# Kernel tuning notes

Measured on AMD Instinct MI355X. Metric: run time of the kernel, lower is better.

## Reference

```python
import jax, jax.numpy as jnp
import numpy as np

BS, SEQ, DIM, DIM_MLP, E = 2, 2048, 1024, 4096, 8
STD = 0.02  # nn.init.normal_(weight, std=0.02)


def setup_inputs() -> dict:
    key = jax.random.key(0)
    k_x, k_idx, k_w1, k_w2 = jax.random.split(key, 4)
    x = jax.random.normal(k_x, (BS, SEQ, DIM), dtype=jnp.float32)
    expert_idx = jax.random.randint(k_idx, (BS, SEQ), 0, E, dtype=jnp.int32)
    W1 = jax.random.normal(k_w1, (E, DIM, DIM_MLP), dtype=jnp.float32) * STD
    b1 = jnp.zeros((E, DIM_MLP), dtype=jnp.float32)
    W2 = jax.random.normal(k_w2, (E, DIM_MLP, DIM), dtype=jnp.float32) * STD
    b2 = jnp.zeros((E, DIM), dtype=jnp.float32)
    return {"x": x, "expert_idx": expert_idx, "W1": W1, "b1": b1, "W2": W2, "b2": b2}


def reference(x, expert_idx, W1, b1, W2, b2):
    # Compute ALL experts on all tokens (faithful to the torch module).
    # h: [bs, seq, E, dim_mlp]
    h = jnp.einsum("bsd,edm->bsem", x, W1) + b1
    h = jax.nn.gelu(h, approximate=False)  # torch nn.GELU default = exact erf
    # feat: [bs, seq, E, dim]  (== torch.cat along feature dim, reshaped)
    feat = jnp.einsum("bsem,emd->bsed", h, W2) + b2
    # Per-token gather of the assigned expert's output (top-1 select).
    idx = expert_idx.astype(jnp.int32)[:, :, None, None]  # [bs, seq, 1, 1]
    out = jnp.take_along_axis(feat, idx, axis=2)[:, :, 0, :]  # [bs, seq, dim]
    return out
```

## Files before the change

kernel.cpp:

```cpp
#include <hip/hip_runtime.h>
#include <hip/hip_bf16.h>
#include <math.h>

#define TOK   4096
#define DIM   1024
#define DMLP  4096
#define NE    8
#define BM    128
#define BN    128
#define BN2   64
#define BK    32
#define PADMAX (TOK + NE * BM)
#define NTILES (PADMAX / BM)

typedef __attribute__((ext_vector_type(8))) short  short8;
typedef __attribute__((ext_vector_type(4))) float  float4v;
typedef __attribute__((ext_vector_type(4))) unsigned short ushort4v;

static __device__ __forceinline__ unsigned short f2bf(float f) {
  unsigned u = __float_as_uint(f);
  u += 0x7fffu + ((u >> 16) & 1u);
  return (unsigned short)(u >> 16);
}

__global__ void group_kernel(const int* __restrict__ eidx,
                             int* __restrict__ perm,
                             int* __restrict__ tile_e) {
  __shared__ int cnt[NE], off[NE], len[NE], cur[NE];
  const int tid = threadIdx.x;
  if (tid < NE) cnt[tid] = 0;
  __syncthreads();
  for (int i = tid; i < TOK; i += 256) atomicAdd(&cnt[eidx[i]], 1);
  __syncthreads();
  if (tid == 0) {
    int o = 0;
    for (int e = 0; e < NE; e++) {
      off[e] = o;
      len[e] = ((cnt[e] + BM - 1) / BM) * BM;
      cur[e] = o;
      o += len[e];
    }
  }
  __syncthreads();
  for (int s = tid; s < PADMAX; s += 256) perm[s] = -1;
  __syncthreads();
  for (int i = tid; i < TOK; i += 256) {
    const int e = eidx[i];
    const int p = atomicAdd(&cur[e], 1);
    perm[p] = i;
  }
  __syncthreads();
  for (int t = tid; t < NTILES; t += 256) {
    const int row = t * BM;
    int te = -1;
    for (int e = 0; e < NE; e++)
      if (row >= off[e] && row < off[e] + len[e]) te = e;
    tile_e[t] = te;
  }
}

__global__ __launch_bounds__(256)
void convtrans_kernel(const float* __restrict__ W, unsigned short* __restrict__ WT,
                      int K, int N) {
  __shared__ unsigned short T[64][66];
  const int e  = blockIdx.z;
  const int k0 = blockIdx.y * 64, n0 = blockIdx.x * 64;
  const float* Win = W + (size_t)e * K * N;
  unsigned short* Wout = WT + (size_t)e * K * N;
  const int tid = threadIdx.x;
  const int nl  = tid & 63;
  const int kb  = (tid >> 6) * 16;
#pragma unroll
  for (int r = 0; r < 16; r++) {
    const int kl = kb + r;
    T[nl][kl] = f2bf(Win[(size_t)(k0 + kl) * N + n0 + nl]);
  }
  __syncthreads();
  const int kc = (tid & 31) * 2;
  const int nb = tid >> 5;
#pragma unroll
  for (int r = 0; r < 8; r++) {
    const int nl2 = nb + r * 8;
    const unsigned v = *(const unsigned*)&T[nl2][kc];
    *(unsigned*)&Wout[(size_t)(n0 + nl2) * K + k0 + kc] = v;
  }
}

__global__ __launch_bounds__(256)
void xgather_kernel(const float* __restrict__ x, const int* __restrict__ perm,
                    unsigned short* __restrict__ xg) {
  const int slot = blockIdx.x;
  const int t    = perm[slot];
  const int tid  = threadIdx.x;
  ushort4v o = (ushort4v){0, 0, 0, 0};
  if (t >= 0) {
    const float4v v = *(const float4v*)(x + (size_t)t * DIM + tid * 4);
#pragma unroll
    for (int q = 0; q < 4; q++) o[q] = f2bf(v[q]);
  }
  *(ushort4v*)(xg + (size_t)slot * DIM + tid * 4) = o;
}

__global__ __launch_bounds__(256, 2)
void gemm1_kernel(const unsigned short* __restrict__ xg,
                  const unsigned short* __restrict__ W1T,
                  const float* __restrict__ b1, const int* __restrict__ tile_e,
                  unsigned short* __restrict__ h) {
  const int te = tile_e[blockIdx.x];
  if (te < 0) return;
  const unsigned short* Bsrc = W1T + (size_t)te * DIM * DMLP;
  const int n0  = blockIdx.y * BN;
  const int tid = threadIdx.x;

  __shared__ unsigned short As[BM][BK + 8];
  __shared__ unsigned short Bs[BN][BK + 8];

  const int srow = tid >> 1;
  const int soff = (tid & 1) * 16;
  const unsigned short* aptr = xg + (size_t)(blockIdx.x * BM + srow) * DIM + soff;
  const unsigned short* bptr = Bsrc + (size_t)(n0 + srow) * DIM + soff;

  const int wid = tid >> 6, lane = tid & 63;
  const int wm = (wid >> 1) * 64, wn = (wid & 1) * 64;
  const int l15 = lane & 15, quad = lane >> 4;

  float4v acc[4][4];
#pragma unroll
  for (int i = 0; i < 4; i++)
#pragma unroll
    for (int j = 0; j < 4; j++) acc[i][j] = (float4v){0.f, 0.f, 0.f, 0.f};

  for (int k0 = 0; k0 < DIM; k0 += BK) {
    const short8 a0 = *(const short8*)(aptr + k0);
    const short8 a1 = *(const short8*)(aptr + k0 + 8);
    const short8 b0 = *(const short8*)(bptr + k0);
    const short8 b1v = *(const short8*)(bptr + k0 + 8);
    *(short8*)&As[srow][soff]     = a0;
    *(short8*)&As[srow][soff + 8] = a1;
    *(short8*)&Bs[srow][soff]     = b0;
    *(short8*)&Bs[srow][soff + 8] = b1v;
    __syncthreads();

    short8 a[4], b[4];
#pragma unroll
    for (int i = 0; i < 4; i++) a[i] = *(short8*)&As[wm + i * 16 + l15][quad * 8];
#pragma unroll
    for (int j = 0; j < 4; j++) b[j] = *(short8*)&Bs[wn + j * 16 + l15][quad * 8];
#pragma unroll
    for (int i = 0; i < 4; i++)
#pragma unroll
      for (int j = 0; j < 4; j++)
        acc[i][j] = __builtin_amdgcn_mfma_f32_16x16x32_bf16(a[i], b[j], acc[i][j], 0, 0, 0);
    __syncthreads();
  }

#pragma unroll
  for (int i = 0; i < 4; i++) {
#pragma unroll
    for (int j = 0; j < 4; j++) {
      const int col = n0 + wn + j * 16 + l15;
      const float bias = b1[te * DMLP + col];
#pragma unroll
      for (int r = 0; r < 4; r++) {
        const int row = wm + i * 16 + quad * 4 + r;
        float v = acc[i][j][r] + bias;
        v = 0.5f * v * (1.0f + erff(v * 0.7071067811865475f));
        h[(size_t)(blockIdx.x * BM + row) * DMLP + col] = f2bf(v);
      }
    }
  }
}

__global__ __launch_bounds__(256, 2)
void gemm2_kernel(const unsigned short* __restrict__ h,
                  const unsigned short* __restrict__ W2T,
                  const float* __restrict__ b2, const int* __restrict__ perm,
                  const int* __restrict__ tile_e, float* __restrict__ out) {
  const int te = tile_e[blockIdx.x];
  if (te < 0) return;
  const unsigned short* Bsrc = W2T + (size_t)te * DMLP * DIM;
  const int n0  = blockIdx.y * BN2;
  const int tid = threadIdx.x;

  __shared__ unsigned short As[BM][BK + 8];
  __shared__ unsigned short Bs[BN2][BK + 8];

  const int arow = tid >> 1;
  const int aoff = (tid & 1) * 16;
  const unsigned short* aptr = h + (size_t)(blockIdx.x * BM + arow) * DMLP + aoff;

  const int brow = tid >> 2;
  const int boff = (tid & 3) * 8;
  const unsigned short* bptr = Bsrc + (size_t)(n0 + brow) * DMLP + boff;

  const int wid = tid >> 6, lane = tid & 63;
  const int wm = (wid >> 1) * 64, wn = (wid & 1) * 32;
  const int l15 = lane & 15, quad = lane >> 4;

  float4v acc[4][2];
#pragma unroll
  for (int i = 0; i < 4; i++)
#pragma unroll
    for (int j = 0; j < 2; j++) acc[i][j] = (float4v){0.f, 0.f, 0.f, 0.f};

  for (int k0 = 0; k0 < DMLP; k0 += BK) {
    const short8 a0 = *(const short8*)(aptr + k0);
    const short8 a1 = *(const short8*)(aptr + k0 + 8);
    const short8 b0 = *(const short8*)(bptr + k0);
    *(short8*)&As[arow][aoff]     = a0;
    *(short8*)&As[arow][aoff + 8] = a1;
    *(short8*)&Bs[brow][boff]     = b0;
    __syncthreads();

    short8 a[4], b[2];
#pragma unroll
    for (int i = 0; i < 4; i++) a[i] = *(short8*)&As[wm + i * 16 + l15][quad * 8];
#pragma unroll
    for (int j = 0; j < 2; j++) b[j] = *(short8*)&Bs[wn + j * 16 + l15][quad * 8];
#pragma unroll
    for (int i = 0; i < 4; i++)
#pragma unroll
      for (int j = 0; j < 2; j++)
        acc[i][j] = __builtin_amdgcn_mfma_f32_16x16x32_bf16(a[i], b[j], acc[i][j], 0, 0, 0);
    __syncthreads();
  }

#pragma unroll
  for (int i = 0; i < 4; i++) {
#pragma unroll
    for (int j = 0; j < 2; j++) {
      const int col = n0 + wn + j * 16 + l15;
      const float bias = b2[te * DIM + col];
#pragma unroll
      for (int r = 0; r < 4; r++) {
        const int row  = wm + i * 16 + quad * 4 + r;
        const int slot = blockIdx.x * BM + row;
        const int t    = perm[slot];
        if (t >= 0) out[(size_t)t * DIM + col] = acc[i][j][r] + bias;
      }
    }
  }
}

extern "C" void kernel_launch(void* const* d_in, const int* in_sizes, int n_in,
                              void* d_out, int out_size, void* d_ws, size_t ws_size,
                              hipStream_t stream) {
  const float* x    = (const float*)d_in[0];
  const int*   eidx = (const int*)d_in[1];
  const float* W1   = (const float*)d_in[2];
  const float* b1   = (const float*)d_in[3];
  const float* W2   = (const float*)d_in[4];
  const float* b2   = (const float*)d_in[5];
  float* out = (float*)d_out;

  char* ws = (char*)d_ws;
  int* perm   = (int*)ws;
  int* tile_e = (int*)(ws + PADMAX * sizeof(int));
  unsigned short* xg  = (unsigned short*)(ws + 32768);
  unsigned short* h   = (unsigned short*)(ws + 32768 + 10485760);
  unsigned short* W1T = (unsigned short*)(ws + 32768 + 10485760 + 41943040);
  unsigned short* W2T = (unsigned short*)((char*)W1T + 67108864);

  group_kernel<<<1, 256, 0, stream>>>(eidx, perm, tile_e);
  convtrans_kernel<<<dim3(DMLP / 64, DIM / 64, NE), 256, 0, stream>>>(W1, W1T, DIM, DMLP);
  convtrans_kernel<<<dim3(DIM / 64, DMLP / 64, NE), 256, 0, stream>>>(W2, W2T, DMLP, DIM);
  xgather_kernel<<<PADMAX, 256, 0, stream>>>(x, perm, xg);
  gemm1_kernel<<<dim3(NTILES, DMLP / BN), 256, 0, stream>>>(xg, W1T, b1, tile_e, h);
  gemm2_kernel<<<dim3(NTILES, DIM / BN2), 256, 0, stream>>>(h, W2T, b2, perm, tile_e, out);
}
```

Baseline: 543.2 us.

## Use direct global-to-LDS async loads with XOR-swizzled tiles and BK=64

Both expert GEMMs now fill shared memory with global_load_lds 16-byte transfers instead of staging through registers. The padded LDS layout is replaced by an XOR-swizzled one to avoid bank conflicts, and the K tile doubles to 64 so each barrier pair covers twice the MFMA work. The occupancy hint of two blocks per CU is dropped. The aim is to cut register pressure and per-iteration sync overhead. The loads are still not double-buffered, and the 16-byte form of global_load_lds depends on gfx950 support.

```diff
diff --git a/kernel.cpp b/kernel.cpp
--- a/kernel.cpp
+++ b/kernel.cpp
@@ -9,13 +9,19 @@
 #define BM    128
 #define BN    128
 #define BN2   64
-#define BK    32
+#define BK    64
 #define PADMAX (TOK + NE * BM)
 #define NTILES (PADMAX / BM)
 
 typedef __attribute__((ext_vector_type(8))) short  short8;
 typedef __attribute__((ext_vector_type(4))) float  float4v;
 typedef __attribute__((ext_vector_type(4))) unsigned short ushort4v;
+
+#define ASYNC16(gp, lp) __builtin_amdgcn_global_load_lds( \
+    (const __attribute__((address_space(1))) unsigned int*)(gp), \
+    (__attribute__((address_space(3))) unsigned int*)(lp), 16, 0, 0)
+
+#define FRAG_OFF(R, C) (((((R) << 3) + ((C) ^ ((R) & 7)))) << 3)
 
 static __device__ __forceinline__ unsigned short f2bf(float f) {
   unsigned u = __float_as_uint(f);
@@ -101,24 +107,32 @@
   *(ushort4v*)(xg + (size_t)slot * DIM + tid * 4) = o;
 }
 
-__global__ __launch_bounds__(256, 2)
+__global__ __launch_bounds__(256)
 void gemm1_kernel(const unsigned short* __restrict__ xg,
                   const unsigned short* __restrict__ W1T,
                   const float* __restrict__ b1, const int* __restrict__ tile_e,
                   unsigned short* __restrict__ h) {
   const int te = tile_e[blockIdx.x];
   if (te < 0) return;
-  const unsigned short* Bsrc = W1T + (size_t)te * DIM * DMLP;
-  const int n0  = blockIdx.y * BN;
-  const int tid = threadIdx.x;
-
-  __shared__ unsigned short As[BM][BK + 8];
-  __shared__ unsigned short Bs[BN][BK + 8];
-
-  const int srow = tid >> 1;
-  const int soff = (tid & 1) * 16;
-  const unsigned short* aptr = xg + (size_t)(blockIdx.x * BM + srow) * DIM + soff;
-  const unsigned short* bptr = Bsrc + (size_t)(n0 + srow) * DIM + soff;
+  const unsigned short* Asrc = xg + (size_t)blockIdx.x * BM * DIM;
+  const unsigned short* Bsrc = W1T + (size_t)te * DIM * DMLP + (size_t)(blockIdx.y * BN) * DIM;
+  const int tid = threadIdx.x;
+
+  __shared__ __align__(16) unsigned short As[BM * BK];
+  __shared__ __align__(16) unsigned short Bs[BN * BK];
+
+  const unsigned short* ag[4];
+  const unsigned short* bg[4];
+  int lo[4];
+#pragma unroll
+  for (int t = 0; t < 4; t++) {
+    const int p = t * 256 + tid;
+    const int r = p >> 3;
+    const int c = (p & 7) ^ (r & 7);
+    ag[t] = Asrc + (size_t)r * DIM + c * 8;
+    bg[t] = Bsrc + (size_t)r * DIM + c * 8;
+    lo[t] = p * 8;
+  }
 
   const int wid = tid >> 6, lane = tid & 63;
   const int wm = (wid >> 1) * 64, wn = (wid & 1) * 64;
@@ -131,26 +145,26 @@
     for (int j = 0; j < 4; j++) acc[i][j] = (float4v){0.f, 0.f, 0.f, 0.f};
 
   for (int k0 = 0; k0 < DIM; k0 += BK) {
-    const short8 a0 = *(const short8*)(aptr + k0);
-    const short8 a1 = *(const short8*)(aptr + k0 + 8);
-    const short8 b0 = *(const short8*)(bptr + k0);
-    const short8 b1v = *(const short8*)(bptr + k0 + 8);
-    *(short8*)&As[srow][soff]     = a0;
-    *(short8*)&As[srow][soff + 8] = a1;
-    *(short8*)&Bs[srow][soff]     = b0;
-    *(short8*)&Bs[srow][soff + 8] = b1v;
-    __syncthreads();
-
-    short8 a[4], b[4];
-#pragma unroll
-    for (int i = 0; i < 4; i++) a[i] = *(short8*)&As[wm + i * 16 + l15][quad * 8];
-#pragma unroll
-    for (int j = 0; j < 4; j++) b[j] = *(short8*)&Bs[wn + j * 16 + l15][quad * 8];
-#pragma unroll
-    for (int i = 0; i < 4; i++)
-#pragma unroll
-      for (int j = 0; j < 4; j++)
-        acc[i][j] = __builtin_amdgcn_mfma_f32_16x16x32_bf16(a[i], b[j], acc[i][j], 0, 0, 0);
+#pragma unroll
+    for (int t = 0; t < 4; t++) ASYNC16(ag[t] + k0, &As[lo[t]]);
+#pragma unroll
+    for (int t = 0; t < 4; t++) ASYNC16(bg[t] + k0, &Bs[lo[t]]);
+    __syncthreads();
+
+#pragma unroll
+    for (int hh = 0; hh < 2; hh++) {
+      short8 a[4], b[4];
+      const int C = hh * 4 + quad;
+#pragma unroll
+      for (int i = 0; i < 4; i++) a[i] = *(const short8*)&As[FRAG_OFF(wm + i * 16 + l15, C)];
+#pragma unroll
+      for (int j = 0; j < 4; j++) b[j] = *(const short8*)&Bs[FRAG_OFF(wn + j * 16 + l15, C)];
+#pragma unroll
+      for (int i = 0; i < 4; i++)
+#pragma unroll
+        for (int j = 0; j < 4; j++)
+          acc[i][j] = __builtin_amdgcn_mfma_f32_16x16x32_bf16(a[i], b[j], acc[i][j], 0, 0, 0);
+    }
     __syncthreads();
   }
 
@@ -158,7 +172,7 @@
   for (int i = 0; i < 4; i++) {
 #pragma unroll
     for (int j = 0; j < 4; j++) {
-      const int col = n0 + wn + j * 16 + l15;
+      const int col = blockIdx.y * BN + wn + j * 16 + l15;
       const float bias = b1[te * DMLP + col];
 #pragma unroll
       for (int r = 0; r < 4; r++) {
@@ -171,27 +185,39 @@
   }
 }
 
-__global__ __launch_bounds__(256, 2)
+__global__ __launch_bounds__(256)
 void gemm2_kernel(const unsigned short* __restrict__ h,
                   const unsigned short* __restrict__ W2T,
                   const float* __restrict__ b2, const int* __restrict__ perm,
                   const int* __restrict__ tile_e, float* __restrict__ out) {
   const int te = tile_e[blockIdx.x];
   if (te < 0) return;
-  const unsigned short* Bsrc = W2T + (size_t)te * DMLP * DIM;
-  const int n0  = blockIdx.y * BN2;
-  const int tid = threadIdx.x;
-
-  __shared__ unsigned short As[BM][BK + 8];
-  __shared__ unsigned short Bs[BN2][BK + 8];
-
-  const int arow = tid >> 1;
-  const int aoff = (tid & 1) * 16;
-  const unsigned short* aptr = h + (size_t)(blockIdx.x * BM + arow) * DMLP + aoff;
-
-  const int brow = tid >> 2;
-  const int boff = (tid & 3) * 8;
-  const unsigned short* bptr = Bsrc + (size_t)(n0 + brow) * DMLP + boff;
+  const unsigned short* Asrc = h + (size_t)blockIdx.x * BM * DMLP;
+  const unsigned short* Bsrc = W2T + (size_t)te * DMLP * DIM + (size_t)(blockIdx.y * BN2) * DMLP;
+  const int tid = threadIdx.x;
+
+  __shared__ __align__(16) unsigned short As[BM * BK];
+  __shared__ __align__(16) unsigned short Bs[BN2 * BK];
+
+  const unsigned short* ag[4];
+  const unsigned short* bg[2];
+  int alo[4], blo[2];
+#pragma unroll
+  for (int t = 0; t < 4; t++) {
+    const int p = t * 256 + tid;
+    const int r = p >> 3;
+    const int c = (p & 7) ^ (r & 7);
+    ag[t] = Asrc + (size_t)r * DMLP + c * 8;
+    alo[t] = p * 8;
+  }
+#pragma unroll
+  for (int t = 0; t < 2; t++) {
+    const int p = t * 256 + tid;
+    const int r = p >> 3;
+    const int c = (p & 7) ^ (r & 7);
+    bg[t] = Bsrc + (size_t)r * DMLP + c * 8;
+    blo[t] = p * 8;
+  }
 
   const int wid = tid >> 6, lane = tid & 63;
   const int wm = (wid >> 1) * 64, wn = (wid & 1) * 32;
@@ -204,24 +230,26 @@
     for (int j = 0; j < 2; j++) acc[i][j] = (float4v){0.f, 0.f, 0.f, 0.f};
 
   for (int k0 = 0; k0 < DMLP; k0 += BK) {
-    const short8 a0 = *(const short8*)(aptr + k0);
-    const short8 a1 = *(const short8*)(aptr + k0 + 8);
-    const short8 b0 = *(const short8*)(bptr + k0);
-    *(short8*)&As[arow][aoff]     = a0;
-    *(short8*)&As[arow][aoff + 8] = a1;
-    *(short8*)&Bs[brow][boff]     = b0;
-    __syncthreads();
-
-    short8 a[4], b[2];
-#pragma unroll
-    for (int i = 0; i < 4; i++) a[i] = *(short8*)&As[wm + i * 16 + l15][quad * 8];
-#pragma unroll
-    for (int j = 0; j < 2; j++) b[j] = *(short8*)&Bs[wn + j * 16 + l15][quad * 8];
-#pragma unroll
-    for (int i = 0; i < 4; i++)
-#pragma unroll
-      for (int j = 0; j < 2; j++)
-        acc[i][j] = __builtin_amdgcn_mfma_f32_16x16x32_bf16(a[i], b[j], acc[i][j], 0, 0, 0);
+#pragma unroll
+    for (int t = 0; t < 4; t++) ASYNC16(ag[t] + k0, &As[alo[t]]);
+#pragma unroll
+    for (int t = 0; t < 2; t++) ASYNC16(bg[t] + k0, &Bs[blo[t]]);
+    __syncthreads();
+
+#pragma unroll
+    for (int hh = 0; hh < 2; hh++) {
+      short8 a[4], b[2];
+      const int C = hh * 4 + quad;
+#pragma unroll
+      for (int i = 0; i < 4; i++) a[i] = *(const short8*)&As[FRAG_OFF(wm + i * 16 + l15, C)];
+#pragma unroll
+      for (int j = 0; j < 2; j++) b[j] = *(const short8*)&Bs[FRAG_OFF(wn + j * 16 + l15, C)];
+#pragma unroll
+      for (int i = 0; i < 4; i++)
+#pragma unroll
+        for (int j = 0; j < 2; j++)
+          acc[i][j] = __builtin_amdgcn_mfma_f32_16x16x32_bf16(a[i], b[j], acc[i][j], 0, 0, 0);
+    }
     __syncthreads();
   }
 
@@ -229,7 +257,7 @@
   for (int i = 0; i < 4; i++) {
 #pragma unroll
     for (int j = 0; j < 2; j++) {
-      const int col = n0 + wn + j * 16 + l15;
+      const int col = blockIdx.y * BN2 + wn + j * 16 + l15;
       const float bias = b2[te * DIM + col];
 #pragma unroll
       for (int r = 0; r < 4; r++) {
```

Measured after the change: 494.3 us. -9.0%, faster.
